# Performance work log

Hardware: AMD Instinct MI355X
Metric: run time of the kernel (lower is better)

Reference implementation:

```python
import jax, jax.numpy as jnp
import numpy as np

B = 4096
STATE_DIM = 64
OBS_DIM = 32
BASE_DEGREE = 8
TIME_STEPS = 96
EPS = 1e-7


def _degree(t):
    # get_degree: degree_params initialized to linspace(0,1,time_steps); used via .item() (static)
    p = float(t) / (TIME_STEPS - 1)
    scaled = 0.5 * (1.0 + np.sin(2.0 * np.pi * p))
    return BASE_DEGREE + int(2.0 * scaled)


def _cheby_fwd_and_jac(x, coeffs, degree):
    """ChebyKAN forward y[b,o] = sum_{i,d} coeffs[i,o,d] * cos(d*acos(clip(tanh(x[b,i]))))
    plus its analytic per-sample Jacobian J[b,o,i] (replaces the torch autograd loop)."""
    t_raw = jnp.tanh(x)                                   # [B, D]
    t_val = jnp.clip(t_raw, -1.0 + EPS, 1.0 - EPS)
    theta = jnp.arccos(t_val)                             # [B, D]
    dvals = jnp.arange(degree + 1, dtype=x.dtype)         # [deg+1]
    ang = theta[..., None] * dvals                        # [B, D, deg+1]
    cheb = jnp.cos(ang)
    ac = coeffs[..., : degree + 1]                        # [D, D, deg+1]
    y = jnp.einsum('bid,iod->bo', cheb, ac)               # [B, D]
    # d cheb / d x = d*sin(d*theta) * (1 - tanh(x)^2) * mask / sqrt(1 - t_val^2)
    mask = ((t_raw > -1.0 + EPS) & (t_raw < 1.0 - EPS)).astype(x.dtype)
    dtheta_dx = -(1.0 - t_raw * t_raw) * mask / jnp.sqrt(1.0 - t_val * t_val)  # [B, D]
    dcheb_dx = -dvals * jnp.sin(ang) * dtheta_dx[..., None]                    # [B, D, deg+1]
    jac = jnp.einsum('bid,iod->boi', dcheb_dx, ac)        # [B, D, D] = dY_o/dx_i
    return y, jac


def setup_inputs() -> dict:
    key = jax.random.key(0)
    ks = jax.random.split(key, 5)
    obs = jax.random.normal(ks[0], (B, OBS_DIM), jnp.float32)
    prev_state = jax.random.normal(ks[1], (B, STATE_DIM), jnp.float32)
    A = jax.random.normal(ks[2], (B, STATE_DIM, STATE_DIM), jnp.float32)
    prev_cov = A @ A.transpose(0, 2, 1) / STATE_DIM + jnp.eye(STATE_DIM, dtype=jnp.float32)  # SPD
    bound = 1.0 / np.sqrt(STATE_DIM * (BASE_DEGREE + 3))  # kaiming-uniform style
    coeffs = jax.random.uniform(ks[3], (STATE_DIM, STATE_DIM, BASE_DEGREE + 3), jnp.float32, -bound, bound)
    M = jax.random.normal(ks[4], (STATE_DIM, OBS_DIM), jnp.float32)
    q, _ = jnp.linalg.qr(M)                               # orthonormal columns
    obs_matrix = q.T.astype(jnp.float32)                  # [OBS_DIM, STATE_DIM], orthogonal rows
    log_Q_diag = jnp.zeros((STATE_DIM,), jnp.float32)
    log_R_diag = jnp.zeros((OBS_DIM,), jnp.float32)
    return dict(obs=obs, prev_state=prev_state, prev_cov=prev_cov, coeffs=coeffs,
                obs_matrix=obs_matrix, log_Q_diag=log_Q_diag, log_R_diag=log_R_diag, t=10)


def reference(obs, prev_state, prev_cov, coeffs, obs_matrix, log_Q_diag, log_R_diag, t):
    degree = _degree(t)
    state_pred, Fj = _cheby_fwd_and_jac(prev_state, coeffs, degree)   # [B,D], [B,D,D]
    q = jnp.exp(log_Q_diag)                                           # [D]
    r = jnp.exp(log_R_diag)                                           # [O]
    H = obs_matrix                                                    # [O, D]
    # cov_pred = F P F^T + Q
    cov_pred = jnp.einsum('bij,bjk,blk->bil', Fj, prev_cov, Fj) + jnp.diag(q)[None]
    obs_pred = state_pred @ H.T                                       # [B, O]
    residual = obs - obs_pred                                         # [B, O]
    # S = H Pp H^T + R
    S = jnp.einsum('ij,bjk,lk->bil', H, cov_pred, H) + jnp.diag(r)[None]
    S_inv = jnp.linalg.pinv(S)                                        # [B, O, O]
    PHt = jnp.einsum('bij,oj->bio', cov_pred, H)                      # [B, D, O]
    K = jnp.einsum('bio,bop->bip', PHt, S_inv)                        # [B, D, O]
    state_update = state_pred + jnp.einsum('bio,bo->bi', K, residual)
    I_KH = jnp.eye(STATE_DIM, dtype=cov_pred.dtype)[None] - jnp.einsum('bio,oj->bij', K, H)
    # Joseph form: (I-KH) Pp (I-KH)^T + K R K^T
    cov_update = (jnp.einsum('bij,bjk,blk->bil', I_KH, cov_pred, I_KH)
                  + jnp.einsum('bio,o,bjo->bij', K, r, K))
    cov_diag = jnp.diagonal(cov_update, axis1=1, axis2=2)
    return state_update, cov_update, cov_diag
```

## Files before the change

kernel.cpp:

```cpp
#include <hip/hip_runtime.h>
#include <math.h>


typedef float f4 __attribute__((ext_vector_type(4)));
typedef float f32x4 __attribute__((ext_vector_type(4)));
typedef short b16x8 __attribute__((ext_vector_type(8)));
typedef short b16x4 __attribute__((ext_vector_type(4)));
typedef unsigned int u32;
typedef unsigned int u32x4 __attribute__((ext_vector_type(4)));
typedef unsigned short u16;

#define EPSC 1e-7f
#define MFMA(a, b, c) __builtin_amdgcn_mfma_f32_16x16x32_bf16(a, b, c, 0, 0, 0)
static constexpr size_t CU_OFF = 4096 * 64;
static constexpr size_t CD_OFF = CU_OFF + 4096ull * 4096;

__device__ __forceinline__ void split2(float x, short &h, short &l) {
  u32 u = __float_as_uint(x);
  h = (short)(u >> 16);
  float rem = x - __uint_as_float(u & 0xffff0000u);
  l = (short)(__float_as_uint(rem) >> 16);
}
__device__ __forceinline__ u32 packsplit(float x) {
  u32 u = __float_as_uint(x) & 0xffff0000u;
  float rem = x - __uint_as_float(u);
  return u | (__float_as_uint(rem) >> 16);
}
__device__ __forceinline__ float unpackf(u32 v) {
  return __uint_as_float(v & 0xffff0000u) + __uint_as_float(v << 16);
}
union U8 { u32x4 u; b16x8 s; };
__device__ __forceinline__ void unpack8(u32x4 q0, u32x4 q1, b16x8 &hi,
                                        b16x8 &lo) {
  U8 H, L;
  H.u[0] = __builtin_amdgcn_perm(q0[1], q0[0], 0x07060302u);
  H.u[1] = __builtin_amdgcn_perm(q0[3], q0[2], 0x07060302u);
  H.u[2] = __builtin_amdgcn_perm(q1[1], q1[0], 0x07060302u);
  H.u[3] = __builtin_amdgcn_perm(q1[3], q1[2], 0x07060302u);
  L.u[0] = __builtin_amdgcn_perm(q0[1], q0[0], 0x05040100u);
  L.u[1] = __builtin_amdgcn_perm(q0[3], q0[2], 0x05040100u);
  L.u[2] = __builtin_amdgcn_perm(q1[1], q1[0], 0x05040100u);
  L.u[3] = __builtin_amdgcn_perm(q1[3], q1[2], 0x05040100u);
  hi = H.s;
  lo = L.s;
}
__device__ __forceinline__ void split8v(f4 a, f4 b, b16x8 &hi, b16x8 &lo) {
#pragma unroll
  for (int j = 0; j < 4; ++j) {
    short hh, ll;
    split2(a[j], hh, ll); hi[j] = hh; lo[j] = ll;
    split2(b[j], hh, ll); hi[4 + j] = hh; lo[4 + j] = ll;
  }
}

__global__ __launch_bounds__(256) void prep_kernel(
    const float *__restrict__ Hm, const float *__restrict__ logQ,
    const float *__restrict__ logR, void *__restrict__ ws) {
  u16 *Hh = (u16 *)ws;
  u16 *Hl = (u16 *)ws + 2048;
  float *wq = (float *)((char *)ws + 8192);
  float *wr = wq + 64;
  const int tid = (int)threadIdx.x;
  f4 a = *(const f4 *)(Hm + tid * 8);
  f4 b = *(const f4 *)(Hm + tid * 8 + 4);
  b16x8 hi, lo;
  split8v(a, b, hi, lo);
  *(b16x8 *)(Hh + tid * 8) = hi;
  *(b16x8 *)(Hl + tid * 8) = lo;
  if (tid < 64) wq[tid] = expf(logQ[tid]);
  else if (tid < 96) wr[tid - 64] = expf(logR[tid - 64]);
}

__global__ __launch_bounds__(256, 4) void kalman_fused(
    const float *__restrict__ obs, const float *__restrict__ prev_state,
    const float *__restrict__ prev_cov, const float *__restrict__ coeffs,
    const float *__restrict__ Hm, const int *__restrict__ tptr,
    const void *__restrict__ ws, float *__restrict__ out) {
  __shared__ __align__(16) unsigned char pool[40704];
  u16 *sPh = (u16 *)(pool);
  u16 *sPl = (u16 *)(pool + 8192);
  u32 *sT = (u32 *)(pool);
  u32 *sPHt = (u32 *)(pool);
  u32 *sK = (u32 *)(pool + 8192);
  u16 *sFh = (u16 *)(pool + 16384);
  u16 *sFl = (u16 *)(pool + 24576);
  u32 *sCov = (u32 *)(pool + 16384);
  float *ypart = (float *)(pool + 32768);
  float *sS = (float *)(pool + 32768);
  float *sChT = (float *)(pool + 33792);
  float *sDcT = (float *)(pool + 36864);
  float *sy = (float *)(pool + 39936);
  float *sresid = (float *)(pool + 40192);
  float *sq = (float *)(pool + 40320);
  float *sr = (float *)(pool + 40576);

  const u16 *wHh = (const u16 *)ws;
  const u16 *wHl = (const u16 *)ws + 2048;
  const float *wq = (const float *)((const char *)ws + 8192);
  const float *wr = wq + 64;

  const int tid = (int)threadIdx.x;
  const int b = (int)blockIdx.x;
  const int w = tid >> 6;
  const int l = tid & 63;
  const int lr = l & 15;
  const int h = l >> 4;

  const int tval = tptr[0];
  const float ang = 6.28318530717958647f * ((float)tval / 95.0f);
  const int D = 9 + (int)(1.0f + sinf(ang));

  {
    const float *Pg = prev_cov + (size_t)b * 4096;
#pragma unroll
    for (int e = 0; e < 4; ++e) {
      const int idx = tid + 256 * e;
      f4 v = *(const f4 *)(Pg + 4 * idx);
      const int r = idx >> 4, c = (idx & 15) * 4;
      const int x = (r & 7) << 3;
      b16x4 h4, l4;
#pragma unroll
      for (int j = 0; j < 4; ++j) {
        short hh, ll;
        split2(v[j], hh, ll);
        h4[j] = hh; l4[j] = ll;
      }
      *(b16x4 *)(sPh + r * 64 + (c ^ x)) = h4;
      *(b16x4 *)(sPl + r * 64 + (c ^ x)) = l4;
    }
    if (tid < 64) {
      sq[tid] = wq[tid];
      const float xx = prev_state[b * 64 + tid];
      const float tr_ = tanhf(xx);
      const float tv = fminf(fmaxf(tr_, -1.0f + EPSC), 1.0f - EPSC);
      const float sn = sqrtf(fmaxf(1.0f - tv * tv, 0.0f));
      const float mask = (tr_ > -1.0f + EPSC && tr_ < 1.0f - EPSC) ? 1.0f : 0.0f;
      const float dth = -(1.0f - tr_ * tr_) * mask / sn;
      float *ct = sChT + tid * 12;
      float *dt = sDcT + tid * 12;
      ct[0] = 1.f; ct[1] = tv; ct[11] = 0.f;
      dt[0] = 0.f; dt[1] = -dth * sn; dt[11] = 0.f;
      float cm2 = 1.f, cm1 = tv, sm2 = 0.f, sm1 = sn;
      const float tv2 = 2.f * tv;
#pragma unroll
      for (int d = 2; d <= 10; ++d) {
        const float cc = fmaf(tv2, cm1, -cm2);
        const float ss = fmaf(tv2, sm1, -sm2);
        ct[d] = (d < D) ? cc : 0.f;
        dt[d] = (d < D) ? (-dth * (float)d * ss) : 0.f;
        cm2 = cm1; cm1 = cc; sm2 = sm1; sm1 = ss;
      }
    } else if (tid < 96) {
      sr[tid - 64] = wr[tid - 64];
    }
  }
  __syncthreads();

  {
    const int o = tid & 63, g = tid >> 6;
    float yacc = 0.f;
    float fr[16];
#pragma unroll
    for (int ii = 0; ii < 16; ++ii) {
      const int i = g * 16 + ii;
      const float *cp = coeffs + (size_t)(i * 64 + o) * 11;
      f4 q0 = *(const f4 *)(cp);
      f4 q1 = *(const f4 *)(cp + 4);
      f4 q2 = *(const f4 *)(cp + 7);
      const float *ct = sChT + i * 12;
      const float *dt = sDcT + i * 12;
      f4 c0 = *(const f4 *)(ct), c1 = *(const f4 *)(ct + 4),
         c2 = *(const f4 *)(ct + 8);
      f4 e0 = *(const f4 *)(dt), e1 = *(const f4 *)(dt + 4),
         e2 = *(const f4 *)(dt + 8);
      float yac = q0[0];
      yac = fmaf(q0[1], c0[1], yac);
      yac = fmaf(q0[2], c0[2], yac);
      yac = fmaf(q0[3], c0[3], yac);
      yac = fmaf(q1[0], c1[0], yac);
      yac = fmaf(q1[1], c1[1], yac);
      yac = fmaf(q1[2], c1[2], yac);
      yac = fmaf(q1[3], c1[3], yac);
      yac = fmaf(q2[1], c2[0], yac);
      yac = fmaf(q2[2], c2[1], yac);
      yac = fmaf(q2[3], c2[2], yac);
      float fra = q0[1] * e0[1];
      fra = fmaf(q0[2], e0[2], fra);
      fra = fmaf(q0[3], e0[3], fra);
      fra = fmaf(q1[0], e1[0], fra);
      fra = fmaf(q1[1], e1[1], fra);
      fra = fmaf(q1[2], e1[2], fra);
      fra = fmaf(q1[3], e1[3], fra);
      fra = fmaf(q2[1], e2[0], fra);
      fra = fmaf(q2[2], e2[1], fra);
      fra = fmaf(q2[3], e2[2], fra);
      yacc += yac;
      fr[ii] = fra;
    }
    b16x8 fh0, fh1, fl0, fl1;
#pragma unroll
    for (int j = 0; j < 8; ++j) {
      short hh, ll;
      split2(fr[j], hh, ll); fh0[j] = hh; fl0[j] = ll;
      split2(fr[8 + j], hh, ll); fh1[j] = hh; fl1[j] = ll;
    }
    const int x = (o & 7) << 3;
    *(b16x8 *)(sFh + o * 64 + ((g * 16) ^ x)) = fh0;
    *(b16x8 *)(sFh + o * 64 + ((g * 16 + 8) ^ x)) = fh1;
    *(b16x8 *)(sFl + o * 64 + ((g * 16) ^ x)) = fl0;
    *(b16x8 *)(sFl + o * 64 + ((g * 16 + 8) ^ x)) = fl1;
    ypart[g * 64 + o] = yacc;
  }
  __syncthreads();

  if (tid < 64) {
    sy[tid] = ypart[tid] + ypart[64 + tid] + ypart[128 + tid] +
              ypart[192 + tid];
  }
  __builtin_amdgcn_wave_barrier();
  if (tid < 32) {
    float racc = obs[b * 32 + tid];
    const float *Hr = Hm + tid * 64;
#pragma unroll
    for (int s = 0; s < 64; s += 4) {
      f4 hv = *(const f4 *)(Hr + s);
      racc -= hv[0] * sy[s] + hv[1] * sy[s + 1] + hv[2] * sy[s + 2] +
              hv[3] * sy[s + 3];
    }
    sresid[tid] = racc;
  }

  f32x4 accT[4] = {{0.f, 0.f, 0.f, 0.f}, {0.f, 0.f, 0.f, 0.f},
                   {0.f, 0.f, 0.f, 0.f}, {0.f, 0.f, 0.f, 0.f}};
  {
    const int m = 16 * w + lr;
    const int xA = (m & 7) << 3;
#pragma unroll
    for (int kc = 0; kc < 2; ++kc) {
      const int k = kc * 32 + h * 8;
      b16x8 Ah = *(const b16x8 *)(sFh + m * 64 + (k ^ xA));
      b16x8 Al = *(const b16x8 *)(sFl + m * 64 + (k ^ xA));
#pragma unroll
      for (int t = 0; t < 4; ++t) {
        const int n = t * 16 + lr;
        const int xB = (n & 7) << 3;
        b16x8 Bh = *(const b16x8 *)(sPh + n * 64 + (k ^ xB));
        b16x8 Bl = *(const b16x8 *)(sPl + n * 64 + (k ^ xB));
        accT[t] = MFMA(Ah, Bh, accT[t]);
        accT[t] = MFMA(Al, Bh, accT[t]);
        accT[t] = MFMA(Ah, Bl, accT[t]);
      }
    }
  }
  __syncthreads();
  {
    const int r0 = 16 * w + h * 4;
#pragma unroll
    for (int t = 0; t < 4; ++t)
#pragma unroll
      for (int j = 0; j < 4; ++j) {
        const int rr = r0 + j, cc = t * 16 + lr;
        sT[rr * 64 + (cc ^ ((rr & 7) << 2))] = packsplit(accT[t][j]);
      }
  }

  f32x4 accC[4] = {{0.f, 0.f, 0.f, 0.f}, {0.f, 0.f, 0.f, 0.f},
                   {0.f, 0.f, 0.f, 0.f}, {0.f, 0.f, 0.f, 0.f}};
  {
    const int m = 16 * w + lr;
    const int xA = (m & 7) << 2;
    const u32 *Tb = sT + m * 64;
#pragma unroll
    for (int kc = 0; kc < 2; ++kc) {
      const int k = kc * 32 + h * 8;
      u32x4 q0 = *(const u32x4 *)(Tb + (k ^ xA));
      u32x4 q1 = *(const u32x4 *)(Tb + ((k + 4) ^ xA));
      b16x8 Ah, Al;
      unpack8(q0, q1, Ah, Al);
#pragma unroll
      for (int t = 0; t < 4; ++t) {
        const int n = t * 16 + lr;
        const int xB = (n & 7) << 3;
        b16x8 Bh = *(const b16x8 *)(sFh + n * 64 + (k ^ xB));
        b16x8 Bl = *(const b16x8 *)(sFl + n * 64 + (k ^ xB));
        accC[t] = MFMA(Ah, Bh, accC[t]);
        accC[t] = MFMA(Al, Bh, accC[t]);
        accC[t] = MFMA(Ah, Bl, accC[t]);
      }
    }
  }
  __syncthreads();
  {
    const int r0 = 16 * w + h * 4;
#pragma unroll
    for (int t = 0; t < 4; ++t)
#pragma unroll
      for (int j = 0; j < 4; ++j) {
        const int rr = r0 + j, cc = t * 16 + lr;
        float v = accC[t][j];
        if (rr == cc) v += sq[rr];
        sCov[rr * 64 + (cc ^ ((rr & 7) << 2))] = packsplit(v);
      }
  }

  {
    f32x4 acc[2] = {{0.f, 0.f, 0.f, 0.f}, {0.f, 0.f, 0.f, 0.f}};
    const int m = 16 * w + lr;
    const int xA = (m & 7) << 2;
    const u32 *Cb = sCov + m * 64;
#pragma unroll
    for (int kc = 0; kc < 2; ++kc) {
      const int k = kc * 32 + h * 8;
      u32x4 q0 = *(const u32x4 *)(Cb + (k ^ xA));
      u32x4 q1 = *(const u32x4 *)(Cb + ((k + 4) ^ xA));
      b16x8 Ah, Al;
      unpack8(q0, q1, Ah, Al);
#pragma unroll
      for (int t = 0; t < 2; ++t) {
        const int n = t * 16 + lr;
        b16x8 Bh = *(const b16x8 *)(wHh + n * 64 + k);
        b16x8 Bl = *(const b16x8 *)(wHl + n * 64 + k);
        acc[t] = MFMA(Ah, Bh, acc[t]);
        acc[t] = MFMA(Al, Bh, acc[t]);
        acc[t] = MFMA(Ah, Bl, acc[t]);
      }
    }
    const int r0 = 16 * w + h * 4;
#pragma unroll
    for (int t = 0; t < 2; ++t)
#pragma unroll
      for (int j = 0; j < 4; ++j) {
        const int rr = r0 + j, cc = t * 16 + lr;
        sPHt[rr * 32 + (cc ^ ((rr & 7) << 2))] = packsplit(acc[t][j]);
      }
  }
  __syncthreads();

  {
    const int tr = w >> 1, tc = w & 1;
    f32x4 acc = {0.f, 0.f, 0.f, 0.f};
    const int m = tr * 16 + lr;
    const int n = tc * 16 + lr;
#pragma unroll
    for (int kc = 0; kc < 2; ++kc) {
      const int k = kc * 32 + h * 8;
      b16x8 Ah = *(const b16x8 *)(wHh + m * 64 + k);
      b16x8 Al = *(const b16x8 *)(wHl + m * 64 + k);
      u32x4 q0, q1;
#pragma unroll
      for (int j = 0; j < 4; ++j)
        q0[j] = sPHt[(k + j) * 32 + (n ^ (j << 2))];
#pragma unroll
      for (int j = 0; j < 4; ++j)
        q1[j] = sPHt[(k + 4 + j) * 32 + (n ^ ((4 + j) << 2))];
      b16x8 Bh, Bl;
      unpack8(q0, q1, Bh, Bl);
      acc = MFMA(Ah, Bh, acc);
      acc = MFMA(Al, Bh, acc);
      acc = MFMA(Ah, Bl, acc);
    }
    const int r0 = tr * 16 + h * 4;
#pragma unroll
    for (int j = 0; j < 4; ++j) {
      const int rr = r0 + j, cc = tc * 16 + lr;
      float v = acc[j];
      if (rr == cc) v += sr[rr];
      sS[rr * 36 + cc] = v;
    }
  }
  __syncthreads();

  if (w == 0) {
    const int mr = l >> 1, half = l & 1;
    float s0[16];
    const float *gbase = sS + mr * 36 + half * 16;
    {
      f4 v0 = *(const f4 *)(gbase + 0), v1 = *(const f4 *)(gbase + 4);
      f4 v2 = *(const f4 *)(gbase + 8), v3 = *(const f4 *)(gbase + 12);
#pragma unroll
      for (int j = 0; j < 4; ++j) {
        s0[j] = v0[j]; s0[4 + j] = v1[j]; s0[8 + j] = v2[j]; s0[12 + j] = v3[j];
      }
    }
#pragma unroll
    for (int p = 0; p < 32; ++p) {
      const int ph = p >> 4, pi = p & 15;
      float prow[16];
#pragma unroll
      for (int j = 0; j < 16; ++j) prow[j] = __shfl(s0[j], 2 * p + half, 64);
      const float dpp = __shfl(s0[pi], 2 * p + ph, 64);
      const float d = 1.0f / dpp;
      const float fv = __shfl(s0[pi], (l & 62) + ph, 64);
      if (mr == p) {
#pragma unroll
        for (int j = 0; j < 16; ++j) s0[j] = prow[j] * d;
        if (half == ph) s0[pi] = d;
      } else {
        const float fd = fv * d;
#pragma unroll
        for (int j = 0; j < 16; ++j) s0[j] = fmaf(-fd, prow[j], s0[j]);
        if (half == ph) s0[pi] = -fd;
      }
    }
    float *wbase = sS + mr * 36 + half * 16;
    f4 w0 = {s0[0], s0[1], s0[2], s0[3]};
    f4 w1 = {s0[4], s0[5], s0[6], s0[7]};
    f4 w2 = {s0[8], s0[9], s0[10], s0[11]};
    f4 w3 = {s0[12], s0[13], s0[14], s0[15]};
    *(f4 *)(wbase + 0) = w0;
    *(f4 *)(wbase + 4) = w1;
    *(f4 *)(wbase + 8) = w2;
    *(f4 *)(wbase + 12) = w3;
  }
  __syncthreads();

  {
    f32x4 acc[2] = {{0.f, 0.f, 0.f, 0.f}, {0.f, 0.f, 0.f, 0.f}};
    const int m = 16 * w + lr;
    const int xA = (m & 7) << 2;
    const int k = h * 8;
    u32x4 q0 = *(const u32x4 *)(sPHt + m * 32 + (k ^ xA));
    u32x4 q1 = *(const u32x4 *)(sPHt + m * 32 + ((k + 4) ^ xA));
    b16x8 Ah, Al;
    unpack8(q0, q1, Ah, Al);
#pragma unroll
    for (int t = 0; t < 2; ++t) {
      const int n = t * 16 + lr;
      f4 b0 = *(const f4 *)(sS + n * 36 + k);
      f4 b1 = *(const f4 *)(sS + n * 36 + k + 4);
      b16x8 Bh, Bl;
      split8v(b0, b1, Bh, Bl);
      acc[t] = MFMA(Ah, Bh, acc[t]);
      acc[t] = MFMA(Al, Bh, acc[t]);
      acc[t] = MFMA(Ah, Bl, acc[t]);
    }
    const int r0 = 16 * w + h * 4;
#pragma unroll
    for (int t = 0; t < 2; ++t)
#pragma unroll
      for (int j = 0; j < 4; ++j) {
        const int rr = r0 + j, cc = t * 16 + lr;
        sK[rr * 32 + (cc ^ ((rr & 7) << 2))] = packsplit(acc[t][j]);
      }
  }
  __syncthreads();

  if (tid < 64) {
    float su = sy[tid];
    const int x = (tid & 7) << 2;
    const u32 *Kb = sK + tid * 32;
#pragma unroll
    for (int c0 = 0; c0 < 32; c0 += 4) {
      u32x4 q = *(const u32x4 *)(Kb + (c0 ^ x));
#pragma unroll
      for (int j = 0; j < 4; ++j)
        su = fmaf(unpackf(q[j]), sresid[c0 + j], su);
    }
    out[b * 64 + tid] = su;
  }
  {
    const int m = 16 * w + lr;
    const int xA = (m & 7) << 2;
    const int k = h * 8;
    u32x4 q0 = *(const u32x4 *)(sK + m * 32 + (k ^ xA));
    u32x4 q1 = *(const u32x4 *)(sK + m * 32 + ((k + 4) ^ xA));
#pragma unroll
    for (int j = 0; j < 4; ++j) {
      q0[j] ^= 0x80008000u;
      q1[j] ^= 0x80008000u;
    }
    b16x8 Ah, Al;
    unpack8(q0, q1, Ah, Al);
    const int r0 = 16 * w + h * 4;
    float *outc = out + CU_OFF + (size_t)b * 4096;
#pragma unroll
    for (int t = 0; t < 4; ++t) {
      const int n = t * 16 + lr;
      const int xB = (n & 7) << 2;
      u32x4 p0 = *(const u32x4 *)(sPHt + n * 32 + (k ^ xB));
      u32x4 p1 = *(const u32x4 *)(sPHt + n * 32 + ((k + 4) ^ xB));
      b16x8 Bh, Bl;
      unpack8(p0, p1, Bh, Bl);
      f32x4 acc;
#pragma unroll
      for (int j = 0; j < 4; ++j) {
        const int rr = r0 + j;
        acc[j] = unpackf(sCov[rr * 64 + (n ^ ((rr & 7) << 2))]);
      }
      acc = MFMA(Ah, Bh, acc);
      acc = MFMA(Al, Bh, acc);
      acc = MFMA(Ah, Bl, acc);
#pragma unroll
      for (int j = 0; j < 4; ++j) {
        const int rr = r0 + j;
        outc[rr * 64 + n] = acc[j];
        if (rr == n) out[CD_OFF + b * 64 + rr] = acc[j];
      }
    }
  }
}

extern "C" void kernel_launch(void *const *d_in, const int *in_sizes, int n_in,
                              void *d_out, int out_size, void *d_ws,
                              size_t ws_size, hipStream_t stream) {
  const float *obs = (const float *)d_in[0];
  const float *prev_state = (const float *)d_in[1];
  const float *prev_cov = (const float *)d_in[2];
  const float *coeffs = (const float *)d_in[3];
  const float *Hm = (const float *)d_in[4];
  const float *logQ = (const float *)d_in[5];
  const float *logR = (const float *)d_in[6];
  const int *tptr = (const int *)d_in[7];
  (void)in_sizes; (void)n_in; (void)out_size; (void)ws_size;
  prep_kernel<<<dim3(1), dim3(256), 0, stream>>>(Hm, logQ, logR, d_ws);
  kalman_fused<<<dim3(4096), dim3(256), 0, stream>>>(
      obs, prev_state, prev_cov, coeffs, Hm, tptr, d_ws, (float *)d_out);
}
```

Before: 121.1 us.

## Use 512 threads per block, splitting each matrix stage across 8 waves

Doubles the block to 8 waves, with each wave owning a 16-row block and half of the output columns in the F·P, T·F^T, P·H^T, K and Joseph-update MFMA stages. The Jacobian computation is spread over 8 groups of 8 inputs, and the shared-memory layout is reshuffled to make room for the extra y partial sums. The goal is more parallelism and latency hiding per batch element. The cost is extra barriers between stages, idle waves in the small S stage, and possible occupancy limits from LDS and registers at 512 threads.

```diff
diff --git a/kernel.cpp b/kernel.cpp
--- a/kernel.cpp
+++ b/kernel.cpp
@@ -71,12 +71,12 @@
   else if (tid < 96) wr[tid - 64] = expf(logR[tid - 64]);
 }
 
-__global__ __launch_bounds__(256, 4) void kalman_fused(
+__global__ __launch_bounds__(512, 8) void kalman_fused(
     const float *__restrict__ obs, const float *__restrict__ prev_state,
     const float *__restrict__ prev_cov, const float *__restrict__ coeffs,
     const float *__restrict__ Hm, const int *__restrict__ tptr,
     const void *__restrict__ ws, float *__restrict__ out) {
-  __shared__ __align__(16) unsigned char pool[40704];
+  __shared__ __align__(16) unsigned char pool[40960];
   u16 *sPh = (u16 *)(pool);
   u16 *sPl = (u16 *)(pool + 8192);
   u32 *sT = (u32 *)(pool);
@@ -85,14 +85,14 @@
   u16 *sFh = (u16 *)(pool + 16384);
   u16 *sFl = (u16 *)(pool + 24576);
   u32 *sCov = (u32 *)(pool + 16384);
-  float *ypart = (float *)(pool + 32768);
-  float *sS = (float *)(pool + 32768);
-  float *sChT = (float *)(pool + 33792);
-  float *sDcT = (float *)(pool + 36864);
-  float *sy = (float *)(pool + 39936);
-  float *sresid = (float *)(pool + 40192);
-  float *sq = (float *)(pool + 40320);
-  float *sr = (float *)(pool + 40576);
+  float *sChT = (float *)(pool + 32768);
+  float *sDcT = (float *)(pool + 35840);
+  float *ypart = (float *)(pool + 38912);
+  float *sy = (float *)(pool + 32768);
+  float *sresid = (float *)(pool + 33024);
+  float *sq = (float *)(pool + 33152);
+  float *sr = (float *)(pool + 33408);
+  float *sS = (float *)(pool + 33536);
 
   const u16 *wHh = (const u16 *)ws;
   const u16 *wHl = (const u16 *)ws + 2048;
@@ -105,16 +105,14 @@
   const int l = tid & 63;
   const int lr = l & 15;
   const int h = l >> 4;
-
-  const int tval = tptr[0];
-  const float ang = 6.28318530717958647f * ((float)tval / 95.0f);
-  const int D = 9 + (int)(1.0f + sinf(ang));
+  const int rb = w >> 1;
+  const int cp = w & 1;
 
   {
     const float *Pg = prev_cov + (size_t)b * 4096;
 #pragma unroll
-    for (int e = 0; e < 4; ++e) {
-      const int idx = tid + 256 * e;
+    for (int e = 0; e < 2; ++e) {
+      const int idx = tid + 512 * e;
       f4 v = *(const f4 *)(Pg + 4 * idx);
       const int r = idx >> 4, c = (idx & 15) * 4;
       const int x = (r & 7) << 3;
@@ -129,7 +127,9 @@
       *(b16x4 *)(sPl + r * 64 + (c ^ x)) = l4;
     }
     if (tid < 64) {
-      sq[tid] = wq[tid];
+      const int tval = tptr[0];
+      const float ang = 6.28318530717958647f * ((float)tval / 95.0f);
+      const int D = 9 + (int)(1.0f + sinf(ang));
       const float xx = prev_state[b * 64 + tid];
       const float tr_ = tanhf(xx);
       const float tv = fminf(fmaxf(tr_, -1.0f + EPSC), 1.0f - EPSC);
@@ -150,23 +150,21 @@
         dt[d] = (d < D) ? (-dth * (float)d * ss) : 0.f;
         cm2 = cm1; cm1 = cc; sm2 = sm1; sm1 = ss;
       }
-    } else if (tid < 96) {
-      sr[tid - 64] = wr[tid - 64];
-    }
-  }
-  __syncthreads();
-
-  {
-    const int o = tid & 63, g = tid >> 6;
+    }
+  }
+  __syncthreads();
+
+  {
+    const int o = tid & 63, g = w;
     float yacc = 0.f;
-    float fr[16];
-#pragma unroll
-    for (int ii = 0; ii < 16; ++ii) {
-      const int i = g * 16 + ii;
-      const float *cp = coeffs + (size_t)(i * 64 + o) * 11;
-      f4 q0 = *(const f4 *)(cp);
-      f4 q1 = *(const f4 *)(cp + 4);
-      f4 q2 = *(const f4 *)(cp + 7);
+    float fr[8];
+#pragma unroll
+    for (int ii = 0; ii < 8; ++ii) {
+      const int i = g * 8 + ii;
+      const float *cp_ = coeffs + (size_t)(i * 64 + o) * 11;
+      f4 q0 = *(const f4 *)(cp_);
+      f4 q1 = *(const f4 *)(cp_ + 4);
+      f4 q2 = *(const f4 *)(cp_ + 7);
       const float *ct = sChT + i * 12;
       const float *dt = sDcT + i * 12;
       f4 c0 = *(const f4 *)(ct), c1 = *(const f4 *)(ct + 4),
@@ -197,25 +195,28 @@
       yacc += yac;
       fr[ii] = fra;
     }
-    b16x8 fh0, fh1, fl0, fl1;
+    b16x8 fh0, fl0;
 #pragma unroll
     for (int j = 0; j < 8; ++j) {
       short hh, ll;
       split2(fr[j], hh, ll); fh0[j] = hh; fl0[j] = ll;
-      split2(fr[8 + j], hh, ll); fh1[j] = hh; fl1[j] = ll;
     }
     const int x = (o & 7) << 3;
-    *(b16x8 *)(sFh + o * 64 + ((g * 16) ^ x)) = fh0;
-    *(b16x8 *)(sFh + o * 64 + ((g * 16 + 8) ^ x)) = fh1;
-    *(b16x8 *)(sFl + o * 64 + ((g * 16) ^ x)) = fl0;
-    *(b16x8 *)(sFl + o * 64 + ((g * 16 + 8) ^ x)) = fl1;
+    *(b16x8 *)(sFh + o * 64 + ((g * 8) ^ x)) = fh0;
+    *(b16x8 *)(sFl + o * 64 + ((g * 8) ^ x)) = fl0;
     ypart[g * 64 + o] = yacc;
   }
   __syncthreads();
 
   if (tid < 64) {
-    sy[tid] = ypart[tid] + ypart[64 + tid] + ypart[128 + tid] +
-              ypart[192 + tid];
+    float s = ypart[tid];
+#pragma unroll
+    for (int g = 1; g < 8; ++g) s += ypart[g * 64 + tid];
+    sy[tid] = s;
+  } else if (tid < 128) {
+    sq[tid - 64] = wq[tid - 64];
+  } else if (tid < 160) {
+    sr[tid - 128] = wr[tid - 128];
   }
   __builtin_amdgcn_wave_barrier();
   if (tid < 32) {
@@ -230,10 +231,9 @@
     sresid[tid] = racc;
   }
 
-  f32x4 accT[4] = {{0.f, 0.f, 0.f, 0.f}, {0.f, 0.f, 0.f, 0.f},
-                   {0.f, 0.f, 0.f, 0.f}, {0.f, 0.f, 0.f, 0.f}};
-  {
-    const int m = 16 * w + lr;
+  f32x4 accT[2] = {{0.f, 0.f, 0.f, 0.f}, {0.f, 0.f, 0.f, 0.f}};
+  {
+    const int m = 16 * rb + lr;
     const int xA = (m & 7) << 3;
 #pragma unroll
     for (int kc = 0; kc < 2; ++kc) {
@@ -241,33 +241,33 @@
       b16x8 Ah = *(const b16x8 *)(sFh + m * 64 + (k ^ xA));
       b16x8 Al = *(const b16x8 *)(sFl + m * 64 + (k ^ xA));
 #pragma unroll
-      for (int t = 0; t < 4; ++t) {
-        const int n = t * 16 + lr;
+      for (int t2 = 0; t2 < 2; ++t2) {
+        const int n = (2 * cp + t2) * 16 + lr;
         const int xB = (n & 7) << 3;
         b16x8 Bh = *(const b16x8 *)(sPh + n * 64 + (k ^ xB));
         b16x8 Bl = *(const b16x8 *)(sPl + n * 64 + (k ^ xB));
-        accT[t] = MFMA(Ah, Bh, accT[t]);
-        accT[t] = MFMA(Al, Bh, accT[t]);
-        accT[t] = MFMA(Ah, Bl, accT[t]);
-      }
-    }
-  }
-  __syncthreads();
-  {
-    const int r0 = 16 * w + h * 4;
-#pragma unroll
-    for (int t = 0; t < 4; ++t)
+        accT[t2] = MFMA(Ah, Bh, accT[t2]);
+        accT[t2] = MFMA(Al, Bh, accT[t2]);
+        accT[t2] = MFMA(Ah, Bl, accT[t2]);
+      }
+    }
+  }
+  __syncthreads();
+  {
+    const int r0 = 16 * rb + h * 4;
+#pragma unroll
+    for (int t2 = 0; t2 < 2; ++t2)
 #pragma unroll
       for (int j = 0; j < 4; ++j) {
-        const int rr = r0 + j, cc = t * 16 + lr;
-        sT[rr * 64 + (cc ^ ((rr & 7) << 2))] = packsplit(accT[t][j]);
-      }
-  }
-
-  f32x4 accC[4] = {{0.f, 0.f, 0.f, 0.f}, {0.f, 0.f, 0.f, 0.f},
-                   {0.f, 0.f, 0.f, 0.f}, {0.f, 0.f, 0.f, 0.f}};
-  {
-    const int m = 16 * w + lr;
+        const int rr = r0 + j, cc = (2 * cp + t2) * 16 + lr;
+        sT[rr * 64 + (cc ^ ((rr & 7) << 2))] = packsplit(accT[t2][j]);
+      }
+  }
+  __syncthreads();
+
+  f32x4 accC[2] = {{0.f, 0.f, 0.f, 0.f}, {0.f, 0.f, 0.f, 0.f}};
+  {
+    const int m = 16 * rb + lr;
     const int xA = (m & 7) << 2;
     const u32 *Tb = sT + m * 64;
 #pragma unroll
@@ -278,36 +278,38 @@
       b16x8 Ah, Al;
       unpack8(q0, q1, Ah, Al);
 #pragma unroll
-      for (int t = 0; t < 4; ++t) {
-        const int n = t * 16 + lr;
+      for (int t2 = 0; t2 < 2; ++t2) {
+        const int n = (2 * cp + t2) * 16 + lr;
         const int xB = (n & 7) << 3;
         b16x8 Bh = *(const b16x8 *)(sFh + n * 64 + (k ^ xB));
         b16x8 Bl = *(const b16x8 *)(sFl + n * 64 + (k ^ xB));
-        accC[t] = MFMA(Ah, Bh, accC[t]);
-        accC[t] = MFMA(Al, Bh, accC[t]);
-        accC[t] = MFMA(Ah, Bl, accC[t]);
-      }
-    }
-  }
-  __syncthreads();
-  {
-    const int r0 = 16 * w + h * 4;
-#pragma unroll
-    for (int t = 0; t < 4; ++t)
+        accC[t2] = MFMA(Ah, Bh, accC[t2]);
+        accC[t2] = MFMA(Al, Bh, accC[t2]);
+        accC[t2] = MFMA(Ah, Bl, accC[t2]);
+      }
+    }
+  }
+  __syncthreads();
+  {
+    const int r0 = 16 * rb + h * 4;
+#pragma unroll
+    for (int t2 = 0; t2 < 2; ++t2)
 #pragma unroll
       for (int j = 0; j < 4; ++j) {
-        const int rr = r0 + j, cc = t * 16 + lr;
-        float v = accC[t][j];
+        const int rr = r0 + j, cc = (2 * cp + t2) * 16 + lr;
+        float v = accC[t2][j];
         if (rr == cc) v += sq[rr];
         sCov[rr * 64 + (cc ^ ((rr & 7) << 2))] = packsplit(v);
       }
   }
-
-  {
-    f32x4 acc[2] = {{0.f, 0.f, 0.f, 0.f}, {0.f, 0.f, 0.f, 0.f}};
-    const int m = 16 * w + lr;
+  __syncthreads();
+
+  {
+    f32x4 acc = {0.f, 0.f, 0.f, 0.f};
+    const int m = 16 * rb + lr;
     const int xA = (m & 7) << 2;
     const u32 *Cb = sCov + m * 64;
+    const int n = cp * 16 + lr;
 #pragma unroll
     for (int kc = 0; kc < 2; ++kc) {
       const int k = kc * 32 + h * 8;
@@ -315,32 +317,25 @@
       u32x4 q1 = *(const u32x4 *)(Cb + ((k + 4) ^ xA));
       b16x8 Ah, Al;
       unpack8(q0, q1, Ah, Al);
-#pragma unroll
-      for (int t = 0; t < 2; ++t) {
-        const int n = t * 16 + lr;
-        b16x8 Bh = *(const b16x8 *)(wHh + n * 64 + k);
-        b16x8 Bl = *(const b16x8 *)(wHl + n * 64 + k);
-        acc[t] = MFMA(Ah, Bh, acc[t]);
-        acc[t] = MFMA(Al, Bh, acc[t]);
-        acc[t] = MFMA(Ah, Bl, acc[t]);
-      }
-    }
-    const int r0 = 16 * w + h * 4;
-#pragma unroll
-    for (int t = 0; t < 2; ++t)
-#pragma unroll
-      for (int j = 0; j < 4; ++j) {
-        const int rr = r0 + j, cc = t * 16 + lr;
-        sPHt[rr * 32 + (cc ^ ((rr & 7) << 2))] = packsplit(acc[t][j]);
-      }
-  }
-  __syncthreads();
-
-  {
-    const int tr = w >> 1, tc = w & 1;
+      b16x8 Bh = *(const b16x8 *)(wHh + n * 64 + k);
+      b16x8 Bl = *(const b16x8 *)(wHl + n * 64 + k);
+      acc = MFMA(Ah, Bh, acc);
+      acc = MFMA(Al, Bh, acc);
+      acc = MFMA(Ah, Bl, acc);
+    }
+    const int r0 = 16 * rb + h * 4;
+#pragma unroll
+    for (int j = 0; j < 4; ++j) {
+      const int rr = r0 + j, cc = cp * 16 + lr;
+      sPHt[rr * 32 + (cc ^ ((rr & 7) << 2))] = packsplit(acc[j]);
+    }
+  }
+  __syncthreads();
+
+  if (w < 4) {
     f32x4 acc = {0.f, 0.f, 0.f, 0.f};
-    const int m = tr * 16 + lr;
-    const int n = tc * 16 + lr;
+    const int m = rb * 16 + lr;
+    const int n = cp * 16 + lr;
 #pragma unroll
     for (int kc = 0; kc < 2; ++kc) {
       const int k = kc * 32 + h * 8;
@@ -359,10 +354,10 @@
       acc = MFMA(Al, Bh, acc);
       acc = MFMA(Ah, Bl, acc);
     }
-    const int r0 = tr * 16 + h * 4;
+    const int r0 = rb * 16 + h * 4;
 #pragma unroll
     for (int j = 0; j < 4; ++j) {
-      const int rr = r0 + j, cc = tc * 16 + lr;
+      const int rr = r0 + j, cc = cp * 16 + lr;
       float v = acc[j];
       if (rr == cc) v += sr[rr];
       sS[rr * 36 + cc] = v;
@@ -415,33 +410,28 @@
   __syncthreads();
 
   {
-    f32x4 acc[2] = {{0.f, 0.f, 0.f, 0.f}, {0.f, 0.f, 0.f, 0.f}};
-    const int m = 16 * w + lr;
+    f32x4 acc = {0.f, 0.f, 0.f, 0.f};
+    const int m = 16 * rb + lr;
     const int xA = (m & 7) << 2;
     const int k = h * 8;
     u32x4 q0 = *(const u32x4 *)(sPHt + m * 32 + (k ^ xA));
     u32x4 q1 = *(const u32x4 *)(sPHt + m * 32 + ((k + 4) ^ xA));
     b16x8 Ah, Al;
     unpack8(q0, q1, Ah, Al);
-#pragma unroll
-    for (int t = 0; t < 2; ++t) {
-      const int n = t * 16 + lr;
-      f4 b0 = *(const f4 *)(sS + n * 36 + k);
-      f4 b1 = *(const f4 *)(sS + n * 36 + k + 4);
-      b16x8 Bh, Bl;
-      split8v(b0, b1, Bh, Bl);
-      acc[t] = MFMA(Ah, Bh, acc[t]);
-      acc[t] = MFMA(Al, Bh, acc[t]);
-      acc[t] = MFMA(Ah, Bl, acc[t]);
-    }
-    const int r0 = 16 * w + h * 4;
-#pragma unroll
-    for (int t = 0; t < 2; ++t)
-#pragma unroll
-      for (int j = 0; j < 4; ++j) {
-        const int rr = r0 + j, cc = t * 16 + lr;
-        sK[rr * 32 + (cc ^ ((rr & 7) << 2))] = packsplit(acc[t][j]);
-      }
+    const int n = cp * 16 + lr;
+    f4 b0 = *(const f4 *)(sS + n * 36 + k);
+    f4 b1 = *(const f4 *)(sS + n * 36 + k + 4);
+    b16x8 Bh, Bl;
+    split8v(b0, b1, Bh, Bl);
+    acc = MFMA(Ah, Bh, acc);
+    acc = MFMA(Al, Bh, acc);
+    acc = MFMA(Ah, Bl, acc);
+    const int r0 = 16 * rb + h * 4;
+#pragma unroll
+    for (int j = 0; j < 4; ++j) {
+      const int rr = r0 + j, cc = cp * 16 + lr;
+      sK[rr * 32 + (cc ^ ((rr & 7) << 2))] = packsplit(acc[j]);
+    }
   }
   __syncthreads();
 
@@ -459,7 +449,7 @@
     out[b * 64 + tid] = su;
   }
   {
-    const int m = 16 * w + lr;
+    const int m = 16 * rb + lr;
     const int xA = (m & 7) << 2;
     const int k = h * 8;
     u32x4 q0 = *(const u32x4 *)(sK + m * 32 + (k ^ xA));
@@ -471,11 +461,11 @@
     }
     b16x8 Ah, Al;
     unpack8(q0, q1, Ah, Al);
-    const int r0 = 16 * w + h * 4;
+    const int r0 = 16 * rb + h * 4;
     float *outc = out + CU_OFF + (size_t)b * 4096;
 #pragma unroll
-    for (int t = 0; t < 4; ++t) {
-      const int n = t * 16 + lr;
+    for (int t2 = 0; t2 < 2; ++t2) {
+      const int n = (2 * cp + t2) * 16 + lr;
       const int xB = (n & 7) << 2;
       u32x4 p0 = *(const u32x4 *)(sPHt + n * 32 + (k ^ xB));
       u32x4 p1 = *(const u32x4 *)(sPHt + n * 32 + ((k + 4) ^ xB));
@@ -513,6 +503,6 @@
   const int *tptr = (const int *)d_in[7];
   (void)in_sizes; (void)n_in; (void)out_size; (void)ws_size;
   prep_kernel<<<dim3(1), dim3(256), 0, stream>>>(Hm, logQ, logR, d_ws);
-  kalman_fused<<<dim3(4096), dim3(256), 0, stream>>>(
+  kalman_fused<<<dim3(4096), dim3(512), 0, stream>>>(
       obs, prev_state, prev_cov, coeffs, Hm, tptr, d_ws, (float *)d_out);
 }
```

Result: slower. 170.1 us (+40.5%).

## Process two batch samples per workgroup to amortize syncs and coefficient loads

Applied to the files above, without the earlier changes.

Each 256-thread block now handles two batch elements, so the grid is halved and the shared pool doubles to 80 KB. Every stage loops over both samples between the same barriers, sharing barrier cost and the coefficient reads and giving each wave more independent MFMA work. In exchange, LDS and register use per block go up and occupancy drops, with launch bounds lowered to 2 blocks per CU.

```diff
diff --git a/kernel.cpp b/kernel.cpp
--- a/kernel.cpp
+++ b/kernel.cpp
@@ -71,47 +71,29 @@
   else if (tid < 96) wr[tid - 64] = expf(logR[tid - 64]);
 }
 
-__global__ __launch_bounds__(256, 4) void kalman_fused(
+__global__ __launch_bounds__(256, 2) void kalman_fused(
     const float *__restrict__ obs, const float *__restrict__ prev_state,
     const float *__restrict__ prev_cov, const float *__restrict__ coeffs,
     const float *__restrict__ Hm, const int *__restrict__ tptr,
     const void *__restrict__ ws, float *__restrict__ out) {
-  __shared__ __align__(16) unsigned char pool[40704];
-  u16 *sPh = (u16 *)(pool);
-  u16 *sPl = (u16 *)(pool + 8192);
-  u32 *sT = (u32 *)(pool);
-  u32 *sPHt = (u32 *)(pool);
-  u32 *sK = (u32 *)(pool + 8192);
-  u16 *sFh = (u16 *)(pool + 16384);
-  u16 *sFl = (u16 *)(pool + 24576);
-  u32 *sCov = (u32 *)(pool + 16384);
-  float *ypart = (float *)(pool + 32768);
-  float *sS = (float *)(pool + 32768);
-  float *sChT = (float *)(pool + 33792);
-  float *sDcT = (float *)(pool + 36864);
-  float *sy = (float *)(pool + 39936);
-  float *sresid = (float *)(pool + 40192);
-  float *sq = (float *)(pool + 40320);
-  float *sr = (float *)(pool + 40576);
-
+  __shared__ __align__(16) unsigned char pool[81920];
   const u16 *wHh = (const u16 *)ws;
   const u16 *wHl = (const u16 *)ws + 2048;
   const float *wq = (const float *)((const char *)ws + 8192);
   const float *wr = wq + 64;
 
   const int tid = (int)threadIdx.x;
-  const int b = (int)blockIdx.x;
+  const int b0 = (int)blockIdx.x * 2;
   const int w = tid >> 6;
   const int l = tid & 63;
   const int lr = l & 15;
   const int h = l >> 4;
 
-  const int tval = tptr[0];
-  const float ang = 6.28318530717958647f * ((float)tval / 95.0f);
-  const int D = 9 + (int)(1.0f + sinf(ang));
-
-  {
-    const float *Pg = prev_cov + (size_t)b * 4096;
+#pragma unroll
+  for (int s = 0; s < 2; ++s) {
+    u16 *sPh = (u16 *)(pool + s * 32768);
+    u16 *sPl = (u16 *)(pool + s * 32768 + 8192);
+    const float *Pg = prev_cov + (size_t)(b0 + s) * 4096;
 #pragma unroll
     for (int e = 0; e < 4; ++e) {
       const int idx = tid + 256 * e;
@@ -128,35 +110,42 @@
       *(b16x4 *)(sPh + r * 64 + (c ^ x)) = h4;
       *(b16x4 *)(sPl + r * 64 + (c ^ x)) = l4;
     }
-    if (tid < 64) {
-      sq[tid] = wq[tid];
-      const float xx = prev_state[b * 64 + tid];
-      const float tr_ = tanhf(xx);
-      const float tv = fminf(fmaxf(tr_, -1.0f + EPSC), 1.0f - EPSC);
-      const float sn = sqrtf(fmaxf(1.0f - tv * tv, 0.0f));
-      const float mask = (tr_ > -1.0f + EPSC && tr_ < 1.0f - EPSC) ? 1.0f : 0.0f;
-      const float dth = -(1.0f - tr_ * tr_) * mask / sn;
-      float *ct = sChT + tid * 12;
-      float *dt = sDcT + tid * 12;
-      ct[0] = 1.f; ct[1] = tv; ct[11] = 0.f;
-      dt[0] = 0.f; dt[1] = -dth * sn; dt[11] = 0.f;
-      float cm2 = 1.f, cm1 = tv, sm2 = 0.f, sm1 = sn;
-      const float tv2 = 2.f * tv;
-#pragma unroll
-      for (int d = 2; d <= 10; ++d) {
-        const float cc = fmaf(tv2, cm1, -cm2);
-        const float ss = fmaf(tv2, sm1, -sm2);
-        ct[d] = (d < D) ? cc : 0.f;
-        dt[d] = (d < D) ? (-dth * (float)d * ss) : 0.f;
-        cm2 = cm1; cm1 = cc; sm2 = sm1; sm1 = ss;
-      }
-    } else if (tid < 96) {
-      sr[tid - 64] = wr[tid - 64];
-    }
-  }
-  __syncthreads();
-
-  {
+  }
+  if (tid < 128) {
+    const int s = tid >> 6, i = tid & 63;
+    float *E = (float *)(pool + 65536 + s * 8192);
+    const int tval = tptr[0];
+    const float ang = 6.28318530717958647f * ((float)tval / 95.0f);
+    const int D = 9 + (int)(1.0f + sinf(ang));
+    const float xx = prev_state[(b0 + s) * 64 + i];
+    const float tr_ = tanhf(xx);
+    const float tv = fminf(fmaxf(tr_, -1.0f + EPSC), 1.0f - EPSC);
+    const float sn = sqrtf(fmaxf(1.0f - tv * tv, 0.0f));
+    const float mask = (tr_ > -1.0f + EPSC && tr_ < 1.0f - EPSC) ? 1.0f : 0.0f;
+    const float dth = -(1.0f - tr_ * tr_) * mask / sn;
+    float *ct = E + i * 12;
+    float *dt = E + 768 + i * 12;
+    ct[0] = 1.f; ct[1] = tv; ct[11] = 0.f;
+    dt[0] = 0.f; dt[1] = -dth * sn; dt[11] = 0.f;
+    float cm2 = 1.f, cm1 = tv, sm2 = 0.f, sm1 = sn;
+    const float tv2 = 2.f * tv;
+#pragma unroll
+    for (int d = 2; d <= 10; ++d) {
+      const float cc = fmaf(tv2, cm1, -cm2);
+      const float ss = fmaf(tv2, sm1, -sm2);
+      ct[d] = (d < D) ? cc : 0.f;
+      dt[d] = (d < D) ? (-dth * (float)d * ss) : 0.f;
+      cm2 = cm1; cm1 = cc; sm2 = sm1; sm1 = ss;
+    }
+  }
+  __syncthreads();
+
+#pragma unroll
+  for (int s = 0; s < 2; ++s) {
+    const float *E = (const float *)(pool + 65536 + s * 8192);
+    u16 *sFh = (u16 *)(pool + s * 32768 + 16384);
+    u16 *sFl = (u16 *)(pool + s * 32768 + 24576);
+    float *ypart = (float *)(pool + 65536 + s * 8192) + 1536;
     const int o = tid & 63, g = tid >> 6;
     float yacc = 0.f;
     float fr[16];
@@ -167,8 +156,8 @@
       f4 q0 = *(const f4 *)(cp);
       f4 q1 = *(const f4 *)(cp + 4);
       f4 q2 = *(const f4 *)(cp + 7);
-      const float *ct = sChT + i * 12;
-      const float *dt = sDcT + i * 12;
+      const float *ct = E + i * 12;
+      const float *dt = E + 768 + i * 12;
       f4 c0 = *(const f4 *)(ct), c1 = *(const f4 *)(ct + 4),
          c2 = *(const f4 *)(ct + 8);
       f4 e0 = *(const f4 *)(dt), e1 = *(const f4 *)(dt + 4),
@@ -214,25 +203,44 @@
   __syncthreads();
 
   if (tid < 64) {
-    sy[tid] = ypart[tid] + ypart[64 + tid] + ypart[128 + tid] +
-              ypart[192 + tid];
+#pragma unroll
+    for (int s = 0; s < 2; ++s) {
+      float *E = (float *)(pool + 65536 + s * 8192);
+      const float *ypart = E + 1536;
+      E[tid] = ypart[tid] + ypart[64 + tid] + ypart[128 + tid] +
+               ypart[192 + tid];
+    }
+  } else if (tid < 192) {
+    const int s = (tid - 64) >> 6, idx = (tid - 64) & 63;
+    float *E = (float *)(pool + 65536 + s * 8192);
+    E[96 + idx] = wq[idx];
+  } else {
+    const int s = (tid - 192) >> 5, idx = (tid - 192) & 31;
+    float *E = (float *)(pool + 65536 + s * 8192);
+    E[160 + idx] = wr[idx];
   }
   __builtin_amdgcn_wave_barrier();
-  if (tid < 32) {
-    float racc = obs[b * 32 + tid];
-    const float *Hr = Hm + tid * 64;
-#pragma unroll
-    for (int s = 0; s < 64; s += 4) {
-      f4 hv = *(const f4 *)(Hr + s);
-      racc -= hv[0] * sy[s] + hv[1] * sy[s + 1] + hv[2] * sy[s + 2] +
-              hv[3] * sy[s + 3];
-    }
-    sresid[tid] = racc;
-  }
-
-  f32x4 accT[4] = {{0.f, 0.f, 0.f, 0.f}, {0.f, 0.f, 0.f, 0.f},
-                   {0.f, 0.f, 0.f, 0.f}, {0.f, 0.f, 0.f, 0.f}};
-  {
+  if (tid < 64) {
+    const int s = l >> 5, r = l & 31;
+    float *E = (float *)(pool + 65536 + s * 8192);
+    float racc = obs[(b0 + s) * 32 + r];
+    const float *Hr = Hm + r * 64;
+#pragma unroll
+    for (int c = 0; c < 64; c += 4) {
+      f4 hv = *(const f4 *)(Hr + c);
+      racc -= hv[0] * E[c] + hv[1] * E[c + 1] + hv[2] * E[c + 2] +
+              hv[3] * E[c + 3];
+    }
+    E[64 + r] = racc;
+  }
+
+  f32x4 accT[2][4] = {};
+#pragma unroll
+  for (int s = 0; s < 2; ++s) {
+    const u16 *sFh = (const u16 *)(pool + s * 32768 + 16384);
+    const u16 *sFl = (const u16 *)(pool + s * 32768 + 24576);
+    const u16 *sPh = (const u16 *)(pool + s * 32768);
+    const u16 *sPl = (const u16 *)(pool + s * 32768 + 8192);
     const int m = 16 * w + lr;
     const int xA = (m & 7) << 3;
 #pragma unroll
@@ -246,27 +254,32 @@
         const int xB = (n & 7) << 3;
         b16x8 Bh = *(const b16x8 *)(sPh + n * 64 + (k ^ xB));
         b16x8 Bl = *(const b16x8 *)(sPl + n * 64 + (k ^ xB));
-        accT[t] = MFMA(Ah, Bh, accT[t]);
-        accT[t] = MFMA(Al, Bh, accT[t]);
-        accT[t] = MFMA(Ah, Bl, accT[t]);
-      }
-    }
-  }
-  __syncthreads();
-  {
+        accT[s][t] = MFMA(Ah, Bh, accT[s][t]);
+        accT[s][t] = MFMA(Al, Bh, accT[s][t]);
+        accT[s][t] = MFMA(Ah, Bl, accT[s][t]);
+      }
+    }
+  }
+  __syncthreads();
+#pragma unroll
+  for (int s = 0; s < 2; ++s) {
+    u32 *sT = (u32 *)(pool + s * 32768);
     const int r0 = 16 * w + h * 4;
 #pragma unroll
     for (int t = 0; t < 4; ++t)
 #pragma unroll
       for (int j = 0; j < 4; ++j) {
         const int rr = r0 + j, cc = t * 16 + lr;
-        sT[rr * 64 + (cc ^ ((rr & 7) << 2))] = packsplit(accT[t][j]);
-      }
-  }
-
-  f32x4 accC[4] = {{0.f, 0.f, 0.f, 0.f}, {0.f, 0.f, 0.f, 0.f},
-                   {0.f, 0.f, 0.f, 0.f}, {0.f, 0.f, 0.f, 0.f}};
-  {
+        sT[rr * 64 + (cc ^ ((rr & 7) << 2))] = packsplit(accT[s][t][j]);
+      }
+  }
+
+  f32x4 accC[2][4] = {};
+#pragma unroll
+  for (int s = 0; s < 2; ++s) {
+    const u32 *sT = (const u32 *)(pool + s * 32768);
+    const u16 *sFh = (const u16 *)(pool + s * 32768 + 16384);
+    const u16 *sFl = (const u16 *)(pool + s * 32768 + 24576);
     const int m = 16 * w + lr;
     const int xA = (m & 7) << 2;
     const u32 *Tb = sT + m * 64;
@@ -283,27 +296,33 @@
         const int xB = (n & 7) << 3;
         b16x8 Bh = *(const b16x8 *)(sFh + n * 64 + (k ^ xB));
         b16x8 Bl = *(const b16x8 *)(sFl + n * 64 + (k ^ xB));
-        accC[t] = MFMA(Ah, Bh, accC[t]);
-        accC[t] = MFMA(Al, Bh, accC[t]);
-        accC[t] = MFMA(Ah, Bl, accC[t]);
-      }
-    }
-  }
-  __syncthreads();
-  {
+        accC[s][t] = MFMA(Ah, Bh, accC[s][t]);
+        accC[s][t] = MFMA(Al, Bh, accC[s][t]);
+        accC[s][t] = MFMA(Ah, Bl, accC[s][t]);
+      }
+    }
+  }
+  __syncthreads();
+#pragma unroll
+  for (int s = 0; s < 2; ++s) {
+    u32 *sCov = (u32 *)(pool + s * 32768 + 16384);
+    const float *E = (const float *)(pool + 65536 + s * 8192);
     const int r0 = 16 * w + h * 4;
 #pragma unroll
     for (int t = 0; t < 4; ++t)
 #pragma unroll
       for (int j = 0; j < 4; ++j) {
         const int rr = r0 + j, cc = t * 16 + lr;
-        float v = accC[t][j];
-        if (rr == cc) v += sq[rr];
+        float v = accC[s][t][j];
+        if (rr == cc) v += E[96 + rr];
         sCov[rr * 64 + (cc ^ ((rr & 7) << 2))] = packsplit(v);
       }
   }
 
-  {
+#pragma unroll
+  for (int s = 0; s < 2; ++s) {
+    const u32 *sCov = (const u32 *)(pool + s * 32768 + 16384);
+    u32 *sPHt = (u32 *)(pool + s * 32768);
     f32x4 acc[2] = {{0.f, 0.f, 0.f, 0.f}, {0.f, 0.f, 0.f, 0.f}};
     const int m = 16 * w + lr;
     const int xA = (m & 7) << 2;
@@ -336,7 +355,10 @@
   }
   __syncthreads();
 
-  {
+#pragma unroll
+  for (int s = 0; s < 2; ++s) {
+    const u32 *sPHt = (const u32 *)(pool + s * 32768);
+    float *E = (float *)(pool + 65536 + s * 8192);
     const int tr = w >> 1, tc = w & 1;
     f32x4 acc = {0.f, 0.f, 0.f, 0.f};
     const int m = tr * 16 + lr;
@@ -364,13 +386,14 @@
     for (int j = 0; j < 4; ++j) {
       const int rr = r0 + j, cc = tc * 16 + lr;
       float v = acc[j];
-      if (rr == cc) v += sr[rr];
-      sS[rr * 36 + cc] = v;
-    }
-  }
-  __syncthreads();
-
-  if (w == 0) {
+      if (rr == cc) v += E[160 + rr];
+      E[192 + rr * 36 + cc] = v;
+    }
+  }
+  __syncthreads();
+
+  if (w < 2) {
+    float *sS = (float *)(pool + 65536 + w * 8192) + 192;
     const int mr = l >> 1, half = l & 1;
     float s0[16];
     const float *gbase = sS + mr * 36 + half * 16;
@@ -414,7 +437,11 @@
   }
   __syncthreads();
 
-  {
+#pragma unroll
+  for (int s = 0; s < 2; ++s) {
+    const u32 *sPHt = (const u32 *)(pool + s * 32768);
+    u32 *sK = (u32 *)(pool + s * 32768 + 8192);
+    const float *sS = (const float *)(pool + 65536 + s * 8192) + 192;
     f32x4 acc[2] = {{0.f, 0.f, 0.f, 0.f}, {0.f, 0.f, 0.f, 0.f}};
     const int m = 16 * w + lr;
     const int xA = (m & 7) << 2;
@@ -445,20 +472,27 @@
   }
   __syncthreads();
 
-  if (tid < 64) {
-    float su = sy[tid];
-    const int x = (tid & 7) << 2;
-    const u32 *Kb = sK + tid * 32;
+  if (tid < 128) {
+    const int s = tid >> 6;
+    const u32 *sK = (const u32 *)(pool + s * 32768 + 8192);
+    const float *E = (const float *)(pool + 65536 + s * 8192);
+    float su = E[l];
+    const int x = (l & 7) << 2;
+    const u32 *Kb = sK + l * 32;
 #pragma unroll
     for (int c0 = 0; c0 < 32; c0 += 4) {
       u32x4 q = *(const u32x4 *)(Kb + (c0 ^ x));
 #pragma unroll
       for (int j = 0; j < 4; ++j)
-        su = fmaf(unpackf(q[j]), sresid[c0 + j], su);
-    }
-    out[b * 64 + tid] = su;
-  }
-  {
+        su = fmaf(unpackf(q[j]), E[64 + c0 + j], su);
+    }
+    out[(b0 + s) * 64 + l] = su;
+  }
+#pragma unroll
+  for (int s = 0; s < 2; ++s) {
+    const u32 *sPHt = (const u32 *)(pool + s * 32768);
+    const u32 *sK = (const u32 *)(pool + s * 32768 + 8192);
+    const u32 *sCov = (const u32 *)(pool + s * 32768 + 16384);
     const int m = 16 * w + lr;
     const int xA = (m & 7) << 2;
     const int k = h * 8;
@@ -472,7 +506,7 @@
     b16x8 Ah, Al;
     unpack8(q0, q1, Ah, Al);
     const int r0 = 16 * w + h * 4;
-    float *outc = out + CU_OFF + (size_t)b * 4096;
+    float *outc = out + CU_OFF + (size_t)(b0 + s) * 4096;
 #pragma unroll
     for (int t = 0; t < 4; ++t) {
       const int n = t * 16 + lr;
@@ -494,7 +528,7 @@
       for (int j = 0; j < 4; ++j) {
         const int rr = r0 + j;
         outc[rr * 64 + n] = acc[j];
-        if (rr == n) out[CD_OFF + b * 64 + rr] = acc[j];
+        if (rr == n) out[CD_OFF + (b0 + s) * 64 + rr] = acc[j];
       }
     }
   }
@@ -513,6 +547,6 @@
   const int *tptr = (const int *)d_in[7];
   (void)in_sizes; (void)n_in; (void)out_size; (void)ws_size;
   prep_kernel<<<dim3(1), dim3(256), 0, stream>>>(Hm, logQ, logR, d_ws);
-  kalman_fused<<<dim3(4096), dim3(256), 0, stream>>>(
+  kalman_fused<<<dim3(2048), dim3(256), 0, stream>>>(
       obs, prev_state, prev_cov, coeffs, Hm, tptr, d_ws, (float *)d_out);
 }
```

Result: slower. 143.2 us (+18.3%).
